# Kernel tuning notes

Hardware: AMD Instinct MI355X
Metric: run time of the kernel (lower is better)

## Reference

```python
import jax, jax.numpy as jnp
import numpy as np

EMBED_DIM = 1024
NUM_HEADS = 16
HEAD_DIM = EMBED_DIM // NUM_HEADS
B, T = 4, 2048


def setup_inputs() -> dict:
    key = jax.random.key(0)
    ks = jax.random.split(key, 11)
    s = 1.0 / np.sqrt(EMBED_DIM)
    return {
        "query": jax.random.normal(ks[0], (B, T, EMBED_DIM), jnp.float32),
        "key_in": jax.random.normal(ks[1], (B, T, EMBED_DIM), jnp.float32),
        "value": jax.random.normal(ks[2], (B, T, EMBED_DIM), jnp.float32),
        "Wq": jax.random.normal(ks[3], (EMBED_DIM, EMBED_DIM), jnp.float32) * s,
        "bq": jnp.zeros((EMBED_DIM,), jnp.float32),
        "Wk": jax.random.normal(ks[4], (EMBED_DIM, EMBED_DIM), jnp.float32) * s,
        "bk": jnp.zeros((EMBED_DIM,), jnp.float32),
        "Wv": jax.random.normal(ks[5], (EMBED_DIM, EMBED_DIM), jnp.float32) * s,
        "bv": jnp.zeros((EMBED_DIM,), jnp.float32),
        "Wo": jax.random.normal(ks[6], (EMBED_DIM, EMBED_DIM), jnp.float32) * s,
        "bo": jnp.zeros((EMBED_DIM,), jnp.float32),
    }


def reference(query, key_in, value, Wq, bq, Wk, bk, Wv, bv, Wo, bo):
    # nn.Linear: x @ W.T + b
    def split_heads(x):  # [B,T,D] -> [B,H,T,hd]
        return x.reshape(B, T, NUM_HEADS, HEAD_DIM).transpose(0, 2, 1, 3)

    q = split_heads(query @ Wq.T + bq)
    k = split_heads(key_in @ Wk.T + bk)
    v = split_heads(value @ Wv.T + bv)
    scores = jnp.einsum("bhqd,bhkd->bhqk", q, k) / jnp.sqrt(jnp.float32(HEAD_DIM))
    attn = jax.nn.softmax(scores, axis=-1)
    out = jnp.einsum("bhqk,bhkd->bhqd", attn, v)
    out = out.transpose(0, 2, 1, 3).reshape(B, T, EMBED_DIM)
    return out @ Wo.T + bo
```

## Files before the change

### kernel.cpp

```cpp
#include <hip/hip_runtime.h>
#include <hip/hip_bf16.h>
#include <stdint.h>

typedef __bf16 bf16;
typedef __bf16 bf16x8 __attribute__((ext_vector_type(8)));
typedef float f32x4 __attribute__((ext_vector_type(4)));
typedef float f32x16 __attribute__((ext_vector_type(16)));

#define BATCH 4
#define SEQ   2048
#define DIM   1024
#define NH    16
#define HD    64

#define QSCALE 0.18033688011112042f

#define MFMA(a, b, c)   __builtin_amdgcn_mfma_f32_16x16x32_bf16((a), (b), (c), 0, 0, 0)
#define MFMA32(a, b, c) __builtin_amdgcn_mfma_f32_32x32x16_bf16((a), (b), (c), 0, 0, 0)

#define GLOAD16(gsrc, ldst)                                                        \
  __builtin_amdgcn_global_load_lds(                                                \
      (__attribute__((address_space(1))) unsigned int*)(void*)(gsrc),              \
      (__attribute__((address_space(3))) unsigned int*)(ldst), 16, 0, 0)

static __device__ __forceinline__ float fast_exp2(float x) {
#if __has_builtin(__builtin_amdgcn_exp2f)
  return __builtin_amdgcn_exp2f(x);
#else
  return exp2f(x);
#endif
}

__global__ __launch_bounds__(256) void cvt_w_kernel(
    const float* __restrict__ w0, const float* __restrict__ w1,
    const float* __restrict__ w2, const float* __restrict__ w3,
    bf16* __restrict__ o0, bf16* __restrict__ o1,
    bf16* __restrict__ o2, bf16* __restrict__ o3) {
  const float* s;
  bf16* d;
  switch (blockIdx.y) {
    case 0: s = w0; d = o0; break;
    case 1: s = w1; d = o1; break;
    case 2: s = w2; d = o2; break;
    default: s = w3; d = o3; break;
  }
  const int i = (blockIdx.x * 256 + threadIdx.x) * 4;
  const float4 v = *(const float4*)(s + i);
  ushort4 o;
  o.x = __builtin_bit_cast(unsigned short, (bf16)v.x);
  o.y = __builtin_bit_cast(unsigned short, (bf16)v.y);
  o.z = __builtin_bit_cast(unsigned short, (bf16)v.z);
  o.w = __builtin_bit_cast(unsigned short, (bf16)v.w);
  *(ushort4*)((unsigned short*)d + i) = o;
}

struct ProjArgs {
  const float* A[3];
  const bf16*  W[3];
  const float* bias[3];
  bf16*        out[3];
};

__global__ __launch_bounds__(256, 3) void proj_gemm(ProjArgs p) {
  const int z = blockIdx.z;
  const float* __restrict__ A    = p.A[z];
  const bf16*  __restrict__ W    = p.W[z];
  const float* __restrict__ bias = p.bias[z];
  bf16*        __restrict__ out  = p.out[z];

  __shared__ float Af[128 * 64];
  __shared__ bf16  Bb[128 * 64];

  const int tid  = threadIdx.x;
  const int wave = tid >> 6, lane = tid & 63;
  const int r = lane & 15, g = lane >> 4;

  const int wg = blockIdx.x;
  const int sw = ((wg & 7) << 6) | (wg >> 3);
  const int m0 = (sw >> 3) * 128, n0 = (sw & 7) * 128;
  const int wm = (wave >> 1) * 64, wn = (wave & 1) * 64;

  f32x4 acc[4][4] = {};

  const int a_sr = lane >> 4;
  const int a_cb = (lane & 15) * 16;
  const int b_sr = lane >> 3;
  const int b_cb = (lane & 7) * 16;

  const int NK = DIM / 64;
  for (int it = 0; it < NK; ++it) {
    const int k0 = it * 64;

#pragma unroll
    for (int i = 0; i < 8; ++i) {
      const int row = wave * 32 + i * 4 + a_sr;
      const char* src = (const char*)(A + (size_t)(m0 + row) * DIM + k0) +
                        (a_cb ^ ((row & 15) << 4));
      GLOAD16(src, (char*)Af + (wave * 32 + i * 4) * 256);
    }
#pragma unroll
    for (int i = 0; i < 4; ++i) {
      const int row = wave * 32 + i * 8 + b_sr;
      const char* src = (const char*)(W + (size_t)(n0 + row) * DIM + k0) +
                        (b_cb ^ ((row & 7) << 4));
      GLOAD16(src, (char*)Bb + (wave * 32 + i * 8) * 128);
    }
    __syncthreads();

#pragma unroll
    for (int ks = 0; ks < 2; ++ks) {
      bf16x8 af[4], bfr[4];
#pragma unroll
      for (int mt = 0; mt < 4; ++mt) {
        const int mr = wm + mt * 16 + r;
        const char* base = (const char*)Af + mr * 256;
        const int asw = (mr & 15) << 4;
        const f32x4 lo = *(const f32x4*)(base + ((ks * 128 + g * 32) ^ asw));
        const f32x4 hi = *(const f32x4*)(base + ((ks * 128 + g * 32 + 16) ^ asw));
        bf16x8 a;
        a[0] = (bf16)lo[0]; a[1] = (bf16)lo[1]; a[2] = (bf16)lo[2]; a[3] = (bf16)lo[3];
        a[4] = (bf16)hi[0]; a[5] = (bf16)hi[1]; a[6] = (bf16)hi[2]; a[7] = (bf16)hi[3];
        af[mt] = a;
      }
#pragma unroll
      for (int nt = 0; nt < 4; ++nt) {
        const int nr = wn + nt * 16 + r;
        bfr[nt] = *(bf16x8*)((char*)Bb + nr * 128 +
                             ((ks * 64 + g * 16) ^ ((nr & 7) << 4)));
      }
#pragma unroll
      for (int mt = 0; mt < 4; ++mt)
#pragma unroll
        for (int nt = 0; nt < 4; ++nt)
          acc[mt][nt] = MFMA(af[mt], bfr[nt], acc[mt][nt]);
    }

    __syncthreads();
  }

  if (z == 2) {
#pragma unroll
    for (int nt = 0; nt < 4; ++nt) {
      const int n = n0 + wn + nt * 16 + r;
      const float bn = bias[n];
#pragma unroll
      for (int mt = 0; mt < 4; ++mt) {
        const int m = m0 + wm + mt * 16 + g * 4;
        const int b = m >> 11, t = m & 2047;
        ushort4 pk;
        pk.x = __builtin_bit_cast(unsigned short, (bf16)(acc[mt][nt][0] + bn));
        pk.y = __builtin_bit_cast(unsigned short, (bf16)(acc[mt][nt][1] + bn));
        pk.z = __builtin_bit_cast(unsigned short, (bf16)(acc[mt][nt][2] + bn));
        pk.w = __builtin_bit_cast(unsigned short, (bf16)(acc[mt][nt][3] + bn));
        *(ushort4*)((unsigned short*)out + (((size_t)(b * DIM + n)) << 11) + t) = pk;
      }
    }
  } else {
    const float scale = (z == 0) ? QSCALE : 1.0f;
#pragma unroll
    for (int mt = 0; mt < 4; ++mt)
#pragma unroll
      for (int nt = 0; nt < 4; ++nt) {
        const int n = n0 + wn + nt * 16 + r;
        const float bn = bias[n];
#pragma unroll
        for (int i = 0; i < 4; ++i) {
          const int m = m0 + wm + mt * 16 + g * 4 + i;
          out[(size_t)m * DIM + n] = (bf16)((acc[mt][nt][i] + bn) * scale);
        }
      }
  }
}

__global__ __launch_bounds__(256, 4) void attn_kernel(
    const bf16* __restrict__ Q, const bf16* __restrict__ K,
    const bf16* __restrict__ Vt, bf16* __restrict__ ctx) {
  __shared__ bf16 Kb[2][64 * 64];
  __shared__ bf16 Vb[2][64 * 64];

  const int tid  = threadIdx.x;
  const int wave = tid >> 6, lane = tid & 63;
  const int l31 = lane & 31, hi = lane >> 5;

  const int wg  = blockIdx.x;
  const int swb = (wg & 7) * 128 + (wg >> 3);
  const int qblk = swb & 15, bh = swb >> 4;
  const int b = bh >> 4, h = bh & 15;
  const int q0 = qblk * 128 + wave * 32;

  bf16x8 qf[4];
  {
    const bf16* qp = Q + ((size_t)(b * SEQ + q0 + l31) * DIM + h * HD);
#pragma unroll
    for (int st = 0; st < 4; ++st)
      qf[st] = *(const bf16x8*)(qp + st * 16 + hi * 8);
  }

  f32x16 accO[2] = {};
  float m_i = -3e38f, l_i = 0.0f;

  const bf16* Kbase = K + (size_t)(b * SEQ) * DIM + h * HD;
  const bf16* Vbase = Vt + (size_t)(b * DIM + h * HD) * SEQ;

  const int srr = lane >> 3;
  const int scb = (lane & 7) * 16;
  const int swz = srr << 4;

  int koff[2], voff[2], kdst[2], vdst[2];
#pragma unroll
  for (int i = 0; i < 2; ++i) {
    const int rl = wave * 16 + i * 8 + srr;
    const int r32 = rl & 31;
    const int t = (r32 >> 2) & 3;
    const int rsrc = (rl & 32) + ((t == 1 || t == 2) ? (r32 ^ 12) : r32);
    koff[i] = rsrc * (DIM * 2) + (scb ^ swz);
    voff[i] = rl * (SEQ * 2) + (scb ^ swz);
    kdst[i] = (wave * 16 + i * 8) * 128;
    vdst[i] = (wave * 16 + i * 8) * 128;
  }

#define STAGE(buf, kv0)                                                             \
  do {                                                                              \
    _Pragma("unroll") for (int i_ = 0; i_ < 2; ++i_) {                              \
      GLOAD16((const char*)Kbase + (size_t)(kv0) * (DIM * 2) + koff[i_],            \
              (char*)&Kb[buf][0] + kdst[i_]);                                       \
      GLOAD16((const char*)Vbase + (size_t)(kv0) * 2 + voff[i_],                    \
              (char*)&Vb[buf][0] + vdst[i_]);                                       \
    }                                                                               \
  } while (0)

  STAGE(0, 0);
  __syncthreads();

  const int NIT = SEQ / 64;
  for (int it = 0; it < NIT; ++it) {
    const int cur = it & 1;
    if (it + 1 < NIT) STAGE(cur ^ 1, (it + 1) * 64);

    f32x16 s[2] = {};
    __builtin_amdgcn_s_setprio(1);
#pragma unroll
    for (int kvt = 0; kvt < 2; ++kvt) {
      const int row = kvt * 32 + l31;
      const char* kb = (const char*)&Kb[cur][0] + row * 128;
      const int rsw = (row & 7) << 4;
#pragma unroll
      for (int st = 0; st < 4; ++st) {
        const bf16x8 kf = *(const bf16x8*)(kb + ((st * 32 + hi * 16) ^ rsw));
        s[kvt] = MFMA32(kf, qf[st], s[kvt]);
      }
    }
    __builtin_amdgcn_s_setprio(0);

    float pm = s[0][0];
#pragma unroll
    for (int kvt = 0; kvt < 2; ++kvt)
#pragma unroll
      for (int e = 0; e < 16; ++e)
        if (kvt || e) pm = fmaxf(pm, s[kvt][e]);
    pm = fmaxf(pm, __shfl_xor(pm, 32));

    if (__any(pm > m_i + 8.0f)) {
      const float mn = fmaxf(m_i, pm);
      const float alpha = fast_exp2(m_i - mn);
      m_i = mn;
      l_i *= alpha;
#pragma unroll
      for (int dt = 0; dt < 2; ++dt)
#pragma unroll
        for (int e = 0; e < 16; ++e) accO[dt][e] *= alpha;
    }

    float rs = 0.0f;
#pragma unroll
    for (int kvt = 0; kvt < 2; ++kvt)
#pragma unroll
      for (int e = 0; e < 16; ++e) {
        s[kvt][e] = fast_exp2(s[kvt][e] - m_i);
        rs += s[kvt][e];
      }
    l_i += rs + __shfl_xor(rs, 32);

    bf16x8 pa[2][2];
#pragma unroll
    for (int kvt = 0; kvt < 2; ++kvt)
#pragma unroll
      for (int kb = 0; kb < 2; ++kb)
#pragma unroll
        for (int j = 0; j < 8; ++j)
          pa[kvt][kb][j] = (bf16)s[kvt][kb * 8 + j];

    __builtin_amdgcn_s_setprio(1);
#pragma unroll
    for (int dt = 0; dt < 2; ++dt) {
      const int row = dt * 32 + l31;
      const char* vb = (const char*)&Vb[cur][0] + row * 128;
      const int rsw = (row & 7) << 4;
#pragma unroll
      for (int kvt = 0; kvt < 2; ++kvt)
#pragma unroll
        for (int kb = 0; kb < 2; ++kb) {
          const bf16x8 vf =
              *(const bf16x8*)(vb + ((kvt * 64 + kb * 32 + hi * 16) ^ rsw));
          accO[dt] = MFMA32(vf, pa[kvt][kb], accO[dt]);
        }
    }
    __builtin_amdgcn_s_setprio(0);

    __syncthreads();
  }
#undef STAGE

  {
    const float inv = 1.0f / l_i;
    bf16* cp = ctx + (size_t)(b * SEQ + q0 + l31) * DIM + h * HD;
#pragma unroll
    for (int dt = 0; dt < 2; ++dt)
#pragma unroll
      for (int rr = 0; rr < 4; ++rr) {
        ushort4 pk;
        pk.x = __builtin_bit_cast(unsigned short, (bf16)(accO[dt][rr * 4 + 0] * inv));
        pk.y = __builtin_bit_cast(unsigned short, (bf16)(accO[dt][rr * 4 + 1] * inv));
        pk.z = __builtin_bit_cast(unsigned short, (bf16)(accO[dt][rr * 4 + 2] * inv));
        pk.w = __builtin_bit_cast(unsigned short, (bf16)(accO[dt][rr * 4 + 3] * inv));
        *(ushort4*)(cp + dt * 32 + rr * 8 + hi * 4) = pk;
      }
  }
}

__global__ __launch_bounds__(256, 2) void out_gemm(
    const bf16* __restrict__ A, const bf16* __restrict__ W,
    const float* __restrict__ bias, float* __restrict__ out) {
  __shared__ bf16 Ab[2][128 * 64];
  __shared__ bf16 Bb[2][128 * 64];

  const int tid  = threadIdx.x;
  const int wave = tid >> 6, lane = tid & 63;
  const int r = lane & 15, g = lane >> 4;

  const int wg = blockIdx.x;
  const int sw = ((wg & 7) << 6) | (wg >> 3);
  const int m0 = (sw >> 3) * 128, n0 = (sw & 7) * 128;
  const int wm = (wave >> 1) * 64, wn = (wave & 1) * 64;

  f32x4 acc[4][4] = {};

  const int srr = lane >> 3;
  const int scb = (lane & 7) * 16;
  const int swz = srr << 4;

#define STAGE2(buf, k0)                                                             \
  do {                                                                              \
    _Pragma("unroll") for (int i_ = 0; i_ < 4; ++i_) {                              \
      const int row_ = wave * 32 + i_ * 8 + srr;                                    \
      const char* as_ =                                                             \
          (const char*)(A + (size_t)(m0 + row_) * DIM + (k0)) + (scb ^ swz);        \
      GLOAD16(as_, (char*)&Ab[buf][0] + (wave * 32 + i_ * 8) * 128);                \
      const char* bs_ =                                                             \
          (const char*)(W + (size_t)(n0 + row_) * DIM + (k0)) + (scb ^ swz);        \
      GLOAD16(bs_, (char*)&Bb[buf][0] + (wave * 32 + i_ * 8) * 128);                \
    }                                                                               \
  } while (0)

  STAGE2(0, 0);
  __syncthreads();

  const int NK = DIM / 64;
  for (int it = 0; it < NK; ++it) {
    const int cur = it & 1;
    if (it + 1 < NK) STAGE2(cur ^ 1, (it + 1) * 64);

#pragma unroll
    for (int ks = 0; ks < 2; ++ks) {
      bf16x8 af[4], bfr[4];
#pragma unroll
      for (int mt = 0; mt < 4; ++mt) {
        const int mr = wm + mt * 16 + r;
        af[mt] = *(bf16x8*)((char*)&Ab[cur][0] + mr * 128 +
                            ((ks * 64 + g * 16) ^ ((mr & 7) << 4)));
      }
#pragma unroll
      for (int nt = 0; nt < 4; ++nt) {
        const int nr = wn + nt * 16 + r;
        bfr[nt] = *(bf16x8*)((char*)&Bb[cur][0] + nr * 128 +
                             ((ks * 64 + g * 16) ^ ((nr & 7) << 4)));
      }
#pragma unroll
      for (int mt = 0; mt < 4; ++mt)
#pragma unroll
        for (int nt = 0; nt < 4; ++nt)
          acc[mt][nt] = MFMA(af[mt], bfr[nt], acc[mt][nt]);
    }

    __syncthreads();
  }
#undef STAGE2

#pragma unroll
  for (int mt = 0; mt < 4; ++mt)
#pragma unroll
    for (int nt = 0; nt < 4; ++nt) {
      const int n = n0 + wn + nt * 16 + r;
      const float bn = bias[n];
#pragma unroll
      for (int i = 0; i < 4; ++i) {
        const int m = m0 + wm + mt * 16 + g * 4 + i;
        out[(size_t)m * DIM + n] = acc[mt][nt][i] + bn;
      }
    }
}

extern "C" void kernel_launch(void* const* d_in, const int* in_sizes, int n_in,
                              void* d_out, int out_size, void* d_ws, size_t ws_size,
                              hipStream_t stream) {
  const float* query  = (const float*)d_in[0];
  const float* key_in = (const float*)d_in[1];
  const float* value  = (const float*)d_in[2];
  const float* Wq = (const float*)d_in[3];
  const float* bq = (const float*)d_in[4];
  const float* Wk = (const float*)d_in[5];
  const float* bk = (const float*)d_in[6];
  const float* Wv = (const float*)d_in[7];
  const float* bv = (const float*)d_in[8];
  const float* Wo = (const float*)d_in[9];
  const float* bo = (const float*)d_in[10];

  char* ws = (char*)d_ws;
  const size_t WSZ = (size_t)DIM * DIM * sizeof(bf16);
  const size_t TSZ = (size_t)BATCH * SEQ * DIM * sizeof(bf16);
  bf16* Wq_b = (bf16*)(ws);
  bf16* Wk_b = (bf16*)(ws + WSZ);
  bf16* Wv_b = (bf16*)(ws + 2 * WSZ);
  bf16* Wo_b = (bf16*)(ws + 3 * WSZ);
  bf16* Q_b  = (bf16*)(ws + 4 * WSZ);
  bf16* K_b  = (bf16*)(ws + 4 * WSZ + TSZ);
  bf16* Vt_b = (bf16*)(ws + 4 * WSZ + 2 * TSZ);
  bf16* C_b  = (bf16*)(ws + 4 * WSZ + 3 * TSZ);

  cvt_w_kernel<<<dim3(DIM * DIM / (256 * 4), 4), 256, 0, stream>>>(
      Wq, Wk, Wv, Wo, Wq_b, Wk_b, Wv_b, Wo_b);

  ProjArgs pa;
  pa.A[0] = query; pa.A[1] = key_in; pa.A[2] = value;
  pa.W[0] = Wq_b;  pa.W[1] = Wk_b;   pa.W[2] = Wv_b;
  pa.bias[0] = bq; pa.bias[1] = bk;  pa.bias[2] = bv;
  pa.out[0] = Q_b; pa.out[1] = K_b;  pa.out[2] = Vt_b;
  proj_gemm<<<dim3(512, 1, 3), 256, 0, stream>>>(pa);

  attn_kernel<<<dim3(1024), 256, 0, stream>>>(Q_b, K_b, Vt_b, C_b);

  out_gemm<<<dim3(512, 1, 1), 256, 0, stream>>>(C_b, Wo_b, bo, (float*)d_out);
}
```

Before: 182.7 us.

## Pre-convert activations to bf16 and double-buffer LDS in projection GEMM

Adds a separate kernel that converts each fp32 activation input to bf16 into a scratch buffer (reusing the context buffer). The projection GEMM then loads bf16 tiles directly and double-buffers LDS, prefetching the next k-tile while computing the current one. The three projections now run as three sequential launches instead of one batched z-grid. This removes in-loop fp32-to-bf16 conversion and halves LDS traffic for A, at the cost of extra global write/read passes over the inputs, more launches, and lower occupancy.

```diff
diff --git a/kernel.cpp b/kernel.cpp
--- a/kernel.cpp
+++ b/kernel.cpp
@@ -54,22 +54,22 @@
   *(ushort4*)((unsigned short*)d + i) = o;
 }
 
-struct ProjArgs {
-  const float* A[3];
-  const bf16*  W[3];
-  const float* bias[3];
-  bf16*        out[3];
-};
-
-__global__ __launch_bounds__(256, 3) void proj_gemm(ProjArgs p) {
-  const int z = blockIdx.z;
-  const float* __restrict__ A    = p.A[z];
-  const bf16*  __restrict__ W    = p.W[z];
-  const float* __restrict__ bias = p.bias[z];
-  bf16*        __restrict__ out  = p.out[z];
-
-  __shared__ float Af[128 * 64];
-  __shared__ bf16  Bb[128 * 64];
+__global__ __launch_bounds__(256) void cvt_x_kernel(
+    const float* __restrict__ in, bf16* __restrict__ out) {
+  const int i = (blockIdx.x * 256 + threadIdx.x) * 8;
+  const float4 v0 = *(const float4*)(in + i);
+  const float4 v1 = *(const float4*)(in + i + 4);
+  bf16x8 p;
+  p[0] = (bf16)v0.x; p[1] = (bf16)v0.y; p[2] = (bf16)v0.z; p[3] = (bf16)v0.w;
+  p[4] = (bf16)v1.x; p[5] = (bf16)v1.y; p[6] = (bf16)v1.z; p[7] = (bf16)v1.w;
+  *(bf16x8*)(out + i) = p;
+}
+
+__global__ __launch_bounds__(256, 2) void proj_gemm(
+    const bf16* __restrict__ A, const bf16* __restrict__ W,
+    const float* __restrict__ bias, bf16* __restrict__ out, int z) {
+  __shared__ bf16 Ab[2][128 * 64];
+  __shared__ bf16 Bb[2][128 * 64];
 
   const int tid  = threadIdx.x;
   const int wave = tid >> 6, lane = tid & 63;
@@ -82,30 +82,30 @@
 
   f32x4 acc[4][4] = {};
 
-  const int a_sr = lane >> 4;
-  const int a_cb = (lane & 15) * 16;
-  const int b_sr = lane >> 3;
-  const int b_cb = (lane & 7) * 16;
+  const int srr = lane >> 3;
+  const int scb = (lane & 7) * 16;
+  const int swz = srr << 4;
+
+#define STAGEP(buf, k0)                                                             \
+  do {                                                                              \
+    _Pragma("unroll") for (int i_ = 0; i_ < 4; ++i_) {                              \
+      const int row_ = wave * 32 + i_ * 8 + srr;                                    \
+      const char* as_ =                                                             \
+          (const char*)(A + (size_t)(m0 + row_) * DIM + (k0)) + (scb ^ swz);        \
+      GLOAD16(as_, (char*)&Ab[buf][0] + (wave * 32 + i_ * 8) * 128);                \
+      const char* bs_ =                                                             \
+          (const char*)(W + (size_t)(n0 + row_) * DIM + (k0)) + (scb ^ swz);        \
+      GLOAD16(bs_, (char*)&Bb[buf][0] + (wave * 32 + i_ * 8) * 128);                \
+    }                                                                               \
+  } while (0)
+
+  STAGEP(0, 0);
+  __syncthreads();
 
   const int NK = DIM / 64;
   for (int it = 0; it < NK; ++it) {
-    const int k0 = it * 64;
-
-#pragma unroll
-    for (int i = 0; i < 8; ++i) {
-      const int row = wave * 32 + i * 4 + a_sr;
-      const char* src = (const char*)(A + (size_t)(m0 + row) * DIM + k0) +
-                        (a_cb ^ ((row & 15) << 4));
-      GLOAD16(src, (char*)Af + (wave * 32 + i * 4) * 256);
-    }
-#pragma unroll
-    for (int i = 0; i < 4; ++i) {
-      const int row = wave * 32 + i * 8 + b_sr;
-      const char* src = (const char*)(W + (size_t)(n0 + row) * DIM + k0) +
-                        (b_cb ^ ((row & 7) << 4));
-      GLOAD16(src, (char*)Bb + (wave * 32 + i * 8) * 128);
-    }
-    __syncthreads();
+    const int cur = it & 1;
+    if (it + 1 < NK) STAGEP(cur ^ 1, (it + 1) * 64);
 
 #pragma unroll
     for (int ks = 0; ks < 2; ++ks) {
@@ -113,19 +113,13 @@
 #pragma unroll
       for (int mt = 0; mt < 4; ++mt) {
         const int mr = wm + mt * 16 + r;
-        const char* base = (const char*)Af + mr * 256;
-        const int asw = (mr & 15) << 4;
-        const f32x4 lo = *(const f32x4*)(base + ((ks * 128 + g * 32) ^ asw));
-        const f32x4 hi = *(const f32x4*)(base + ((ks * 128 + g * 32 + 16) ^ asw));
-        bf16x8 a;
-        a[0] = (bf16)lo[0]; a[1] = (bf16)lo[1]; a[2] = (bf16)lo[2]; a[3] = (bf16)lo[3];
-        a[4] = (bf16)hi[0]; a[5] = (bf16)hi[1]; a[6] = (bf16)hi[2]; a[7] = (bf16)hi[3];
-        af[mt] = a;
+        af[mt] = *(bf16x8*)((char*)&Ab[cur][0] + mr * 128 +
+                            ((ks * 64 + g * 16) ^ ((mr & 7) << 4)));
       }
 #pragma unroll
       for (int nt = 0; nt < 4; ++nt) {
         const int nr = wn + nt * 16 + r;
-        bfr[nt] = *(bf16x8*)((char*)Bb + nr * 128 +
+        bfr[nt] = *(bf16x8*)((char*)&Bb[cur][0] + nr * 128 +
                              ((ks * 64 + g * 16) ^ ((nr & 7) << 4)));
       }
 #pragma unroll
@@ -137,6 +131,7 @@
 
     __syncthreads();
   }
+#undef STAGEP
 
   if (z == 2) {
 #pragma unroll
@@ -436,18 +431,23 @@
   bf16* K_b  = (bf16*)(ws + 4 * WSZ + TSZ);
   bf16* Vt_b = (bf16*)(ws + 4 * WSZ + 2 * TSZ);
   bf16* C_b  = (bf16*)(ws + 4 * WSZ + 3 * TSZ);
+  bf16* X_b  = C_b;
 
   cvt_w_kernel<<<dim3(DIM * DIM / (256 * 4), 4), 256, 0, stream>>>(
       Wq, Wk, Wv, Wo, Wq_b, Wk_b, Wv_b, Wo_b);
 
-  ProjArgs pa;
-  pa.A[0] = query; pa.A[1] = key_in; pa.A[2] = value;
-  pa.W[0] = Wq_b;  pa.W[1] = Wk_b;   pa.W[2] = Wv_b;
-  pa.bias[0] = bq; pa.bias[1] = bk;  pa.bias[2] = bv;
-  pa.out[0] = Q_b; pa.out[1] = K_b;  pa.out[2] = Vt_b;
-  proj_gemm<<<dim3(512, 1, 3), 256, 0, stream>>>(pa);
+  const int XBLK = BATCH * SEQ * DIM / (256 * 8);
+
+  cvt_x_kernel<<<dim3(XBLK), 256, 0, stream>>>(query, X_b);
+  proj_gemm<<<dim3(512), 256, 0, stream>>>(X_b, Wq_b, bq, Q_b, 0);
+
+  cvt_x_kernel<<<dim3(XBLK), 256, 0, stream>>>(key_in, X_b);
+  proj_gemm<<<dim3(512), 256, 0, stream>>>(X_b, Wk_b, bk, K_b, 1);
+
+  cvt_x_kernel<<<dim3(XBLK), 256, 0, stream>>>(value, X_b);
+  proj_gemm<<<dim3(512), 256, 0, stream>>>(X_b, Wv_b, bv, Vt_b, 2);
 
   attn_kernel<<<dim3(1024), 256, 0, stream>>>(Q_b, K_b, Vt_b, C_b);
 
-  out_gemm<<<dim3(512, 1, 1), 256, 0, stream>>>(C_b, Wo_b, bo, (float*)d_out);
-}
+  out_gemm<<<dim3(512), 256, 0, stream>>>(C_b, Wo_b, bo, (float*)d_out);
+}
```

Measured after the change: 208.1 us. 13.9% more time.

## Store K/V tiles in LDS in MFMA-fragment order and tree-reduce softmax max/sum

Applied to the files above, without the earlier changes.

K and V tiles are now staged into LDS in the exact per-lane MFMA operand layout, with each 1 KB block holding one fragment for all 64 lanes. Every lane then reads a contiguous 16 bytes at lane*16, which removes the XOR swizzle address math and aims for conflict-free ds_read_b128. The global loads become 16-byte chunks scattered across 32 rows per wave instruction, which may hurt global coalescing. The row max and row sum are also rewritten as balanced trees to shorten their dependency chains.

```diff
diff --git a/kernel.cpp b/kernel.cpp
--- a/kernel.cpp
+++ b/kernel.cpp
@@ -175,8 +175,8 @@
 __global__ __launch_bounds__(256, 4) void attn_kernel(
     const bf16* __restrict__ Q, const bf16* __restrict__ K,
     const bf16* __restrict__ Vt, bf16* __restrict__ ctx) {
-  __shared__ bf16 Kb[2][64 * 64];
-  __shared__ bf16 Vb[2][64 * 64];
+  __shared__ alignas(16) char Kl[2 * 8192];
+  __shared__ alignas(16) char Vl[2 * 8192];
 
   const int tid  = threadIdx.x;
   const int wave = tid >> 6, lane = tid & 63;
@@ -199,33 +199,32 @@
   f32x16 accO[2] = {};
   float m_i = -3e38f, l_i = 0.0f;
 
-  const bf16* Kbase = K + (size_t)(b * SEQ) * DIM + h * HD;
-  const bf16* Vbase = Vt + (size_t)(b * DIM + h * HD) * SEQ;
-
-  const int srr = lane >> 3;
-  const int scb = (lane & 7) * 16;
-  const int swz = srr << 4;
-
-  int koff[2], voff[2], kdst[2], vdst[2];
+  const char* Kbase = (const char*)(K + (size_t)(b * SEQ) * DIM + h * HD);
+  const char* Vbase = (const char*)(Vt + (size_t)(b * DIM + h * HD) * SEQ);
+
+  const int t_ = (l31 >> 2) & 3;
+  const int pl = (t_ == 1 || t_ == 2) ? (l31 ^ 12) : l31;
+
+  int ksrc[2], kdst[2], vsrc[2], vdst[2];
 #pragma unroll
   for (int i = 0; i < 2; ++i) {
-    const int rl = wave * 16 + i * 8 + srr;
-    const int r32 = rl & 31;
-    const int t = (r32 >> 2) & 3;
-    const int rsrc = (rl & 32) + ((t == 1 || t == 2) ? (r32 ^ 12) : r32);
-    koff[i] = rsrc * (DIM * 2) + (scb ^ swz);
-    voff[i] = rl * (SEQ * 2) + (scb ^ swz);
-    kdst[i] = (wave * 16 + i * 8) * 128;
-    vdst[i] = (wave * 16 + i * 8) * 128;
+    const int ka = wave * 2 + i;
+    const int kvt = ka >> 2, st = ka & 3;
+    ksrc[i] = ((kvt * 32 + pl) * DIM + st * 16 + hi * 8) * 2;
+    kdst[i] = ka * 1024;
+    const int va = wave * 2 + i;
+    const int dt = va >> 2, kvt2 = (va >> 1) & 1, kb = va & 1;
+    vsrc[i] = ((dt * 32 + l31) * SEQ + kvt2 * 32 + kb * 16 + hi * 8) * 2;
+    vdst[i] = va * 1024;
   }
 
 #define STAGE(buf, kv0)                                                             \
   do {                                                                              \
     _Pragma("unroll") for (int i_ = 0; i_ < 2; ++i_) {                              \
-      GLOAD16((const char*)Kbase + (size_t)(kv0) * (DIM * 2) + koff[i_],            \
-              (char*)&Kb[buf][0] + kdst[i_]);                                       \
-      GLOAD16((const char*)Vbase + (size_t)(kv0) * 2 + voff[i_],                    \
-              (char*)&Vb[buf][0] + vdst[i_]);                                       \
+      GLOAD16(Kbase + (size_t)(kv0) * (2 * DIM) + ksrc[i_],                         \
+              Kl + (buf) * 8192 + kdst[i_]);                                        \
+      GLOAD16(Vbase + (size_t)(kv0) * 2 + vsrc[i_],                                 \
+              Vl + (buf) * 8192 + vdst[i_]);                                        \
     }                                                                               \
   } while (0)
 
@@ -237,28 +236,30 @@
     const int cur = it & 1;
     if (it + 1 < NIT) STAGE(cur ^ 1, (it + 1) * 64);
 
+    const char* kbp = Kl + cur * 8192 + lane * 16;
     f32x16 s[2] = {};
     __builtin_amdgcn_s_setprio(1);
 #pragma unroll
-    for (int kvt = 0; kvt < 2; ++kvt) {
-      const int row = kvt * 32 + l31;
-      const char* kb = (const char*)&Kb[cur][0] + row * 128;
-      const int rsw = (row & 7) << 4;
+    for (int kvt = 0; kvt < 2; ++kvt)
 #pragma unroll
       for (int st = 0; st < 4; ++st) {
-        const bf16x8 kf = *(const bf16x8*)(kb + ((st * 32 + hi * 16) ^ rsw));
+        const bf16x8 kf = *(const bf16x8*)(kbp + (kvt * 4 + st) * 1024);
         s[kvt] = MFMA32(kf, qf[st], s[kvt]);
       }
-    }
     __builtin_amdgcn_s_setprio(0);
 
-    float pm = s[0][0];
-#pragma unroll
-    for (int kvt = 0; kvt < 2; ++kvt)
-#pragma unroll
-      for (int e = 0; e < 16; ++e)
-        if (kvt || e) pm = fmaxf(pm, s[kvt][e]);
-    pm = fmaxf(pm, __shfl_xor(pm, 32));
+    float pm;
+    {
+      f32x16 m16;
+#pragma unroll
+      for (int e = 0; e < 16; ++e) m16[e] = fmaxf(s[0][e], s[1][e]);
+      f32x4 m4;
+#pragma unroll
+      for (int e = 0; e < 4; ++e)
+        m4[e] = fmaxf(fmaxf(m16[e], m16[e + 4]), fmaxf(m16[e + 8], m16[e + 12]));
+      pm = fmaxf(fmaxf(m4[0], m4[1]), fmaxf(m4[2], m4[3]));
+      pm = fmaxf(pm, __shfl_xor(pm, 32));
+    }
 
     if (__any(pm > m_i + 8.0f)) {
       const float mn = fmaxf(m_i, pm);
@@ -271,15 +272,21 @@
         for (int e = 0; e < 16; ++e) accO[dt][e] *= alpha;
     }
 
-    float rs = 0.0f;
 #pragma unroll
     for (int kvt = 0; kvt < 2; ++kvt)
 #pragma unroll
-      for (int e = 0; e < 16; ++e) {
-        s[kvt][e] = fast_exp2(s[kvt][e] - m_i);
-        rs += s[kvt][e];
-      }
-    l_i += rs + __shfl_xor(rs, 32);
+      for (int e = 0; e < 16; ++e) s[kvt][e] = fast_exp2(s[kvt][e] - m_i);
+    {
+      f32x16 t16;
+#pragma unroll
+      for (int e = 0; e < 16; ++e) t16[e] = s[0][e] + s[1][e];
+      f32x4 t4;
+#pragma unroll
+      for (int e = 0; e < 4; ++e)
+        t4[e] = (t16[e] + t16[e + 4]) + (t16[e + 8] + t16[e + 12]);
+      float rs = (t4[0] + t4[1]) + (t4[2] + t4[3]);
+      l_i += rs + __shfl_xor(rs, 32);
+    }
 
     bf16x8 pa[2][2];
 #pragma unroll
@@ -290,21 +297,18 @@
         for (int j = 0; j < 8; ++j)
           pa[kvt][kb][j] = (bf16)s[kvt][kb * 8 + j];
 
+    const char* vbp = Vl + cur * 8192 + lane * 16;
     __builtin_amdgcn_s_setprio(1);
 #pragma unroll
-    for (int dt = 0; dt < 2; ++dt) {
-      const int row = dt * 32 + l31;
-      const char* vb = (const char*)&Vb[cur][0] + row * 128;
-      const int rsw = (row & 7) << 4;
+    for (int dt = 0; dt < 2; ++dt)
 #pragma unroll
       for (int kvt = 0; kvt < 2; ++kvt)
 #pragma unroll
         for (int kb = 0; kb < 2; ++kb) {
           const bf16x8 vf =
-              *(const bf16x8*)(vb + ((kvt * 64 + kb * 32 + hi * 16) ^ rsw));
+              *(const bf16x8*)(vbp + (dt * 4 + kvt * 2 + kb) * 1024);
           accO[dt] = MFMA32(vf, pa[kvt][kb], accO[dt]);
         }
-    }
     __builtin_amdgcn_s_setprio(0);
 
     __syncthreads();
@@ -449,5 +453,5 @@
 
   attn_kernel<<<dim3(1024), 256, 0, stream>>>(Q_b, K_b, Vt_b, C_b);
 
-  out_gemm<<<dim3(512, 1, 1), 256, 0, stream>>>(C_b, Wo_b, bo, (float*)d_out);
-}
+  out_gemm<<<dim3(512), 256, 0, stream>>>(C_b, Wo_b, bo, (float*)d_out);
+}
```

New measurement: 193.3 us. +5.8%, slower.
